# Optimization experiments

Hardware: AMD Instinct MI355X
Metric: run time of the kernel (lower is better)

Reference implementation:

```python
import jax, jax.numpy as jnp
import numpy as np

D_MODEL = 768
D_STATE = 128
D_CONV = 4
EXPAND = 2
HEADDIM = 64
NGROUPS = 1
D_INNER = EXPAND * D_MODEL            # 1536
NHEADS = D_INNER // HEADDIM           # 24
CONV_DIM = D_INNER + 2 * NGROUPS * D_STATE  # 1792
D_IN_PROJ = 2 * D_INNER + 2 * NGROUPS * D_STATE + NHEADS  # 3352
EPS = 1e-5


def setup_inputs() -> dict:
    key = jax.random.key(0)
    ks = jax.random.split(key, 8)
    b, l = 4, 2048
    return {
        "feature": jax.random.normal(ks[0], (b, l, D_MODEL), jnp.float32),
        "in_proj_w": jax.random.normal(ks[1], (D_IN_PROJ, D_MODEL), jnp.float32) * 0.02,
        "conv_w": jax.random.normal(ks[2], (CONV_DIM, D_CONV), jnp.float32) * 0.2,
        "conv_b": jnp.zeros((CONV_DIM,), jnp.float32),
        "dt_bias": jax.random.normal(ks[3], (NHEADS,), jnp.float32) * 0.1,
        # A in [1,16) -> A_log = log(A)
        "A_log": jnp.log(1.0 + 15.0 * jax.random.uniform(ks[4], (NHEADS,), jnp.float32)),
        "D": jnp.ones((NHEADS,), jnp.float32),
        "norm_w": jnp.ones((D_INNER,), jnp.float32),
        "out_proj_w": jax.random.normal(ks[5], (D_MODEL, D_INNER), jnp.float32) * 0.02,
        "gate1": jnp.float32(0.6),
    }


def _mamba2(u, in_proj_w, conv_w, conv_b, dt_bias, A_log, D, norm_w, out_proj_w):
    b, l, _ = u.shape
    zxbcdt = jnp.einsum('bld,ed->ble', u, in_proj_w)  # [b,l,3352]
    z, xBC, dt = jnp.split(zxbcdt, [D_INNER, D_INNER + CONV_DIM], axis=-1)
    dt = jax.nn.softplus(dt + dt_bias)  # [b,l,h]

    # causal depthwise conv1d + silu on xBC
    xc = jnp.transpose(xBC, (0, 2, 1))  # [b,c,l]
    xc = jax.lax.conv_general_dilated(
        xc, conv_w[:, None, :], (1,), [(D_CONV - 1, 0)],
        dimension_numbers=('NCH', 'OIH', 'NCH'), feature_group_count=CONV_DIM)
    xBC = jax.nn.silu(jnp.transpose(xc, (0, 2, 1)) + conv_b)

    x, B, C = jnp.split(xBC, [D_INNER, D_INNER + NGROUPS * D_STATE], axis=-1)
    x = x.reshape(b, l, NHEADS, HEADDIM)
    A = -jnp.exp(A_log)          # [h], negative
    dA = jnp.exp(dt * A)         # [b,l,h]

    def step(h, inp):
        # h: [b,h,p,n]
        dA_t, dt_t, x_t, B_t, C_t = inp  # [b,h],[b,h],[b,h,p],[b,n],[b,n]
        h = h * dA_t[..., None, None] + (dt_t[..., None] * x_t)[..., None] * B_t[:, None, None, :]
        y = jnp.einsum('bhpn,bn->bhp', h, C_t)
        return h, y

    h0 = jnp.zeros((b, NHEADS, HEADDIM, D_STATE), u.dtype)
    xs = (jnp.moveaxis(dA, 1, 0), jnp.moveaxis(dt, 1, 0), jnp.moveaxis(x, 1, 0),
          jnp.moveaxis(B, 1, 0), jnp.moveaxis(C, 1, 0))
    _, ys = jax.lax.scan(step, h0, xs)           # [l,b,h,p]
    y = jnp.moveaxis(ys, 0, 1) + x * D[None, None, :, None]
    y = y.reshape(b, l, D_INNER)

    # gated RMSNorm: gate then normalize (norm_before_gate=False)
    y = y * jax.nn.silu(z)
    y = y * jax.lax.rsqrt(jnp.mean(y * y, axis=-1, keepdims=True) + EPS) * norm_w
    return jnp.einsum('bld,ed->ble', y, out_proj_w)


def reference(feature, in_proj_w, conv_w, conv_b, dt_bias, A_log, D, norm_w, out_proj_w, gate1):
    out = _mamba2(feature, in_proj_w, conv_w, conv_b, dt_bias, A_log, D, norm_w, out_proj_w)
    return jax.nn.sigmoid(gate1) * out
```

## Files before the change

### kernel.cpp

```cpp
#include <hip/hip_runtime.h>
#include <cstddef>

#define NB 4
#define SEQL 2048
#define DMODEL 768
#define DSTATE 128
#define HEADDIM 64
#define NHEADS 24
#define DINNER 1536
#define CONVDIM 1792
#define DINPROJ 3352
#define BLROWS (NB*SEQL)
#define RMS_EPS 1e-5f
#define Q 128
#define NC (SEQL/Q)
#define BOFF DINNER
#define COFF (DINNER + DSTATE)
#define BK 64

typedef unsigned int uint;
typedef unsigned short ushort;
typedef __attribute__((ext_vector_type(8))) short bf16x8;
typedef __attribute__((ext_vector_type(4))) float f32x4;

__device__ __forceinline__ float fexp_(float x){ return __expf(x); }
__device__ __forceinline__ float sigmoidf_(float x){ return 1.f/(1.f+__expf(-x)); }
__device__ __forceinline__ float siluf_(float x){ return x * sigmoidf_(x); }
__device__ __forceinline__ float softplusf_(float x){ return x > 20.f ? x : log1pf(__expf(x)); }

__device__ __forceinline__ ushort f2bf(float f){
    union { float f; uint u; } v; v.f = f;
    uint r = (v.u + 0x7FFFu + ((v.u >> 16) & 1u)) >> 16;
    return (ushort)r;
}
__device__ __forceinline__ float bf2f(ushort s){
    union { uint u; float f; } v; v.u = ((uint)s) << 16;
    return v.f;
}
__device__ __forceinline__ uint pack2(float a, float b){
    return (uint)f2bf(a) | ((uint)f2bf(b) << 16);
}
__device__ __forceinline__ void unpack8(uint4 r, float* o){
    o[0]=bf2f((ushort)(r.x&0xffff)); o[1]=bf2f((ushort)(r.x>>16));
    o[2]=bf2f((ushort)(r.y&0xffff)); o[3]=bf2f((ushort)(r.y>>16));
    o[4]=bf2f((ushort)(r.z&0xffff)); o[5]=bf2f((ushort)(r.z>>16));
    o[6]=bf2f((ushort)(r.w&0xffff)); o[7]=bf2f((ushort)(r.w>>16));
}
__device__ __forceinline__ uint packu2(ushort a, ushort b){
    return (uint)a | ((uint)b << 16);
}

#define GLD16(g, l) __builtin_amdgcn_global_load_lds( \
    (const __attribute__((address_space(1))) void*)(g), \
    (__attribute__((address_space(3))) void*)(l), 16, 0, 0)

#define MFMA_BF16(a, b, c) __builtin_amdgcn_mfma_f32_16x16x32_bf16((a), (b), (c), 0, 0, 0)

__global__ __launch_bounds__(256) void cast2_kernel(
    const float* __restrict__ a, ushort* __restrict__ oa, int n4a,
    const float* __restrict__ b, ushort* __restrict__ ob, int n4b)
{
    const int i = blockIdx.x*256 + threadIdx.x;
    if (i < n4a) {
        float4 v = ((const float4*)a)[i];
        ((ushort4*)oa)[i] = make_ushort4(f2bf(v.x), f2bf(v.y), f2bf(v.z), f2bf(v.w));
    } else {
        const int j = i - n4a;
        if (j < n4b) {
            float4 v = ((const float4*)b)[j];
            ((ushort4*)ob)[j] = make_ushort4(f2bf(v.x), f2bf(v.y), f2bf(v.z), f2bf(v.w));
        }
    }
}

__global__ __launch_bounds__(256) void gemm_mfma(
    const ushort* __restrict__ A, const ushort* __restrict__ W,
    float* __restrict__ C, int M, int N, int K,
    const float* __restrict__ gptr)
{
    __shared__ __align__(16) ushort sm[2*12288];
    const int tid = threadIdx.x;
    const int wv = tid >> 6, ln = tid & 63;
    const int id = blockIdx.x;
    const int xcd = id & 7;
    const int local = id >> 3;
    const int m0 = (xcd*8 + (local & 7)) * 128;
    const int n0 = (local >> 3) * 64;
    const int wm = (wv >> 1) * 64, wn = (wv & 1) * 32;

    const int sr = ln >> 3;
    const int scol = ((ln & 7) ^ sr) * 8;
    const ushort* gA[4]; ushort* lA[4];
#pragma unroll
    for (int iss = 0; iss < 4; ++iss) {
        gA[iss] = A + (size_t)(m0 + wv*32 + iss*8 + sr) * K + scol;
        lA[iss] = &sm[(wv*32 + iss*8) * BK];
    }
    const ushort* gB[2]; ushort* lB[2];
#pragma unroll
    for (int iss = 0; iss < 2; ++iss) {
        gB[iss] = W + (size_t)(n0 + wv*16 + iss*8 + sr) * K + scol;
        lB[iss] = &sm[8192 + (wv*16 + iss*8) * BK];
    }

    f32x4 acc[4][2];
#pragma unroll
    for (int i = 0; i < 4; ++i)
#pragma unroll
        for (int j = 0; j < 2; ++j) acc[i][j] = (f32x4){0.f, 0.f, 0.f, 0.f};

    const int fr = ln & 15;
    const int fq = ln >> 4;
    const int nt = K / BK;

#pragma unroll
    for (int iss = 0; iss < 4; ++iss) GLD16(gA[iss], lA[iss]);
#pragma unroll
    for (int iss = 0; iss < 2; ++iss) GLD16(gB[iss], lB[iss]);

    for (int kt = 0; kt < nt; ++kt) {
        if (kt + 1 < nt) {
            const int so = ((kt + 1) & 1) * 12288;
            const int ko = (kt + 1) * BK;
#pragma unroll
            for (int iss = 0; iss < 4; ++iss) GLD16(gA[iss] + ko, lA[iss] + so);
#pragma unroll
            for (int iss = 0; iss < 2; ++iss) GLD16(gB[iss] + ko, lB[iss] + so);
            asm volatile("s_waitcnt vmcnt(6)" ::: "memory");
        } else {
            asm volatile("s_waitcnt vmcnt(0)" ::: "memory");
        }
        __builtin_amdgcn_s_barrier();
        const ushort* As = sm + (kt & 1) * 12288;
        const ushort* Bs = As + 8192;
#pragma unroll
        for (int kh = 0; kh < 2; ++kh) {
            const int sw = ((kh*4 + fq) ^ (fr & 7)) * 8;
            bf16x8 af[4], bfr[2];
#pragma unroll
            for (int i = 0; i < 4; ++i)
                af[i] = *(const bf16x8*)&As[(wm + i*16 + fr)*BK + sw];
#pragma unroll
            for (int j = 0; j < 2; ++j)
                bfr[j] = *(const bf16x8*)&Bs[(wn + j*16 + fr)*BK + sw];
#pragma unroll
            for (int i = 0; i < 4; ++i)
#pragma unroll
                for (int j = 0; j < 2; ++j)
                    acc[i][j] = MFMA_BF16(af[i], bfr[j], acc[i][j]);
        }
        __builtin_amdgcn_s_barrier();
    }

    float scale = 1.f;
    if (gptr) scale = sigmoidf_(*gptr);
    const int cn = ln & 15;
    const int cr = (ln >> 4) * 4;
#pragma unroll
    for (int i = 0; i < 4; ++i) {
        const int mb = m0 + wm + i*16 + cr;
#pragma unroll
        for (int j = 0; j < 2; ++j) {
            const int n = n0 + wn + j*16 + cn;
            if (n < N) {
                float* cp = C + (size_t)mb * N + n;
                cp[0*(size_t)N] = acc[i][j].x * scale;
                cp[1*(size_t)N] = acc[i][j].y * scale;
                cp[2*(size_t)N] = acc[i][j].z * scale;
                cp[3*(size_t)N] = acc[i][j].w * scale;
            }
        }
    }
}

__global__ __launch_bounds__(256) void gemm_mfma_bf16o(
    const ushort* __restrict__ A, const ushort* __restrict__ W,
    ushort* __restrict__ C, float* __restrict__ dtraw, int M, int N, int K)
{
    __shared__ __align__(16) ushort sm[2*128*BK*2];
    const int tid = threadIdx.x;
    const int wv = tid >> 6, ln = tid & 63;
    const int id = blockIdx.x;
    const int xcd = id & 7;
    const int local = id >> 3;
    const int m0 = (xcd*8 + (local & 7)) * 128;
    const int n0 = (local >> 3) * 128;
    const int wm = (wv >> 1) * 64, wn = (wv & 1) * 64;

    const int sr = ln >> 3;
    const int scol = ((ln & 7) ^ sr) * 8;
    const ushort* gA[4]; const ushort* gB[4];
    ushort* lA[4]; ushort* lB[4];
#pragma unroll
    for (int iss = 0; iss < 4; ++iss) {
        const int ra = m0 + wv*32 + iss*8 + sr;
        gA[iss] = A + (size_t)ra * K + scol;
        int rb = n0 + wv*32 + iss*8 + sr; if (rb >= N) rb = N - 1;
        gB[iss] = W + (size_t)rb * K + scol;
        lA[iss] = &sm[(wv*32 + iss*8) * BK];
        lB[iss] = &sm[8192 + (wv*32 + iss*8) * BK];
    }

    f32x4 acc[4][4];
#pragma unroll
    for (int i = 0; i < 4; ++i)
#pragma unroll
        for (int j = 0; j < 4; ++j) acc[i][j] = (f32x4){0.f, 0.f, 0.f, 0.f};

    const int fr = ln & 15;
    const int fq = ln >> 4;
    const int nt = K / BK;

#pragma unroll
    for (int iss = 0; iss < 4; ++iss) {
        GLD16(gA[iss], lA[iss]);
        GLD16(gB[iss], lB[iss]);
    }

    for (int kt = 0; kt < nt; ++kt) {
        if (kt + 1 < nt) {
            const int so = ((kt + 1) & 1) * 16384;
            const int ko = (kt + 1) * BK;
#pragma unroll
            for (int iss = 0; iss < 4; ++iss) {
                GLD16(gA[iss] + ko, lA[iss] + so);
                GLD16(gB[iss] + ko, lB[iss] + so);
            }
            asm volatile("s_waitcnt vmcnt(8)" ::: "memory");
        } else {
            asm volatile("s_waitcnt vmcnt(0)" ::: "memory");
        }
        __builtin_amdgcn_s_barrier();
        const ushort* As = sm + (kt & 1) * 16384;
        const ushort* Bs = As + 8192;
#pragma unroll
        for (int kh = 0; kh < 2; ++kh) {
            const int sw = ((kh*4 + fq) ^ (fr & 7)) * 8;
            bf16x8 af[4], bfr[4];
#pragma unroll
            for (int i = 0; i < 4; ++i)
                af[i] = *(const bf16x8*)&As[(wm + i*16 + fr)*BK + sw];
#pragma unroll
            for (int j = 0; j < 4; ++j)
                bfr[j] = *(const bf16x8*)&Bs[(wn + j*16 + fr)*BK + sw];
#pragma unroll
            for (int i = 0; i < 4; ++i)
#pragma unroll
                for (int j = 0; j < 4; ++j)
                    acc[i][j] = MFMA_BF16(af[i], bfr[j], acc[i][j]);
        }
        __builtin_amdgcn_s_barrier();
    }

    const int cn = ln & 15;
    const int cr = (ln >> 4) * 4;
    __syncthreads();
    ushort* rp = sm + wv*4096;
#pragma unroll
    for (int i = 0; i < 4; ++i)
#pragma unroll
        for (int j = 0; j < 4; ++j) {
            const int colb = j*16 + cn;
#pragma unroll
            for (int r = 0; r < 4; ++r) {
                const int row = i*16 + cr + r;
                rp[row*64 + (((colb >> 3) ^ (row & 7)) * 8) + (colb & 7)] = f2bf(acc[i][j][r]);
            }
        }
    __syncthreads();
#pragma unroll
    for (int k2 = 0; k2 < 8; ++k2) {
        const int row = k2*8 + (ln >> 3);
        const int cg = ln & 7;
        uint4 v = *(const uint4*)&rp[row*64 + ((cg ^ (row & 7)) * 8)];
        const int gm = m0 + wm + row;
        const int gn = n0 + wn + cg*8;
        if (gn + 8 <= N)
            *(uint4*)(C + (size_t)gm*N + gn) = v;
    }
    if (n0 + 128 > N) {
#pragma unroll
        for (int i = 0; i < 4; ++i) {
            const int mb = m0 + wm + i*16 + cr;
#pragma unroll
            for (int j = 0; j < 4; ++j) {
                const int col = (n0 + wn + j*16 + cn) - (N - 24);
                if (col >= 0 && col < 24) {
                    dtraw[(size_t)(mb+0)*24 + col] = acc[i][j].x;
                    dtraw[(size_t)(mb+1)*24 + col] = acc[i][j].y;
                    dtraw[(size_t)(mb+2)*24 + col] = acc[i][j].z;
                    dtraw[(size_t)(mb+3)*24 + col] = acc[i][j].w;
                }
            }
        }
    }
}

__global__ __launch_bounds__(448) void conv_dtscan_kernel(
    const ushort* __restrict__ zx, const float* __restrict__ conv_w,
    const float* __restrict__ conv_b, ushort* __restrict__ xconv,
    const float* __restrict__ dtraw, const float* __restrict__ dt_bias,
    const float* __restrict__ A_log, float* __restrict__ dtc,
    float* __restrict__ clog)
{
    if (blockIdx.x < BLROWS/16) {
        const int c4 = threadIdx.x;
        const int bl0 = blockIdx.x * 16;
        const int l0 = bl0 & (SEQL - 1);
        float w[4][4];
#pragma unroll
        for (int j = 0; j < 4; ++j) {
            float4 wr = *(const float4*)(conv_w + (c4*4 + j)*4);
            w[j][0]=wr.x; w[j][1]=wr.y; w[j][2]=wr.z; w[j][3]=wr.w;
        }
        const float4 bias = *(const float4*)(conv_b + c4*4);
        const ushort* src = zx + DINNER + (size_t)c4*4;
        ushort* dst = xconv + (size_t)c4*4;

        float h0[4], h1[4], h2[4];
        if (l0 == 0) {
#pragma unroll
            for (int ch = 0; ch < 4; ++ch) { h0[ch]=0.f; h1[ch]=0.f; h2[ch]=0.f; }
        } else {
            ushort4 a = *(const ushort4*)(src + (size_t)(bl0-3)*DINPROJ);
            ushort4 b = *(const ushort4*)(src + (size_t)(bl0-2)*DINPROJ);
            ushort4 c = *(const ushort4*)(src + (size_t)(bl0-1)*DINPROJ);
            h0[0]=bf2f(a.x); h0[1]=bf2f(a.y); h0[2]=bf2f(a.z); h0[3]=bf2f(a.w);
            h1[0]=bf2f(b.x); h1[1]=bf2f(b.y); h1[2]=bf2f(b.z); h1[3]=bf2f(b.w);
            h2[0]=bf2f(c.x); h2[1]=bf2f(c.y); h2[2]=bf2f(c.z); h2[3]=bf2f(c.w);
        }
#pragma unroll
        for (int t = 0; t < 16; ++t) {
            ushort4 xv = *(const ushort4*)(src + (size_t)(bl0 + t)*DINPROJ);
            float h3[4] = {bf2f(xv.x), bf2f(xv.y), bf2f(xv.z), bf2f(xv.w)};
            float s0 = fmaf(h3[0], w[0][3], fmaf(h2[0], w[0][2], fmaf(h1[0], w[0][1], fmaf(h0[0], w[0][0], bias.x))));
            float s1 = fmaf(h3[1], w[1][3], fmaf(h2[1], w[1][2], fmaf(h1[1], w[1][1], fmaf(h0[1], w[1][0], bias.y))));
            float s2 = fmaf(h3[2], w[2][3], fmaf(h2[2], w[2][2], fmaf(h1[2], w[2][1], fmaf(h0[2], w[2][0], bias.z))));
            float s3 = fmaf(h3[3], w[3][3], fmaf(h2[3], w[3][2], fmaf(h1[3], w[3][1], fmaf(h0[3], w[3][0], bias.w))));
            ushort4 o = make_ushort4(f2bf(siluf_(s0)), f2bf(siluf_(s1)),
                                     f2bf(siluf_(s2)), f2bf(siluf_(s3)));
            *(ushort4*)(dst + (size_t)(bl0 + t)*CONVDIM) = o;
#pragma unroll
            for (int ch = 0; ch < 4; ++ch) { h0[ch]=h1[ch]; h1[ch]=h2[ch]; h2[ch]=h3[ch]; }
        }
    } else {
        const int id = blockIdx.x - BLROWS/16;
        const int c = id & (NC - 1);
        const int h = (id >> 4) % NHEADS;
        const int b = id / (NC * NHEADS);
        const int t = threadIdx.x;
        __shared__ float w0tot;
        float v = 0.f, dtv = 0.f;
        if (t < 128) {
            const int bl = b*SEQL + c*Q + t;
            float draw = dtraw[(size_t)bl*24 + h] + dt_bias[h];
            dtv = softplusf_(draw);
            v = -fexp_(A_log[h]) * dtv;
            const int lane = t & 63;
#pragma unroll
            for (int off = 1; off < 64; off <<= 1) {
                float u = __shfl_up(v, off);
                if (lane >= off) v += u;
            }
            if (t == 63) w0tot = v;
        }
        __syncthreads();
        if (t < 128) {
            if (t >= 64) v += w0tot;
            const int idx = (b*NHEADS + h)*SEQL + c*Q + t;
            dtc[idx] = dtv;
            clog[idx] = v;
        }
    }
}

#define ASTR 40
#define BSTR 40
__global__ __launch_bounds__(256) void gcb_locstate_kernel(
    const ushort* __restrict__ xconv, ushort* __restrict__ G,
    const float* __restrict__ dtc, const float* __restrict__ clog,
    ushort* __restrict__ Sloc)
{
    __shared__ __align__(16) char smraw[15872];
    const int tid = threadIdx.x;
    const int wv = tid >> 6, ln = tid & 63;
    const int fr = ln & 15, fq = ln >> 4, fk = fq*8;

    if (blockIdx.x < 2*NC*NB) {
        ushort* Ca = (ushort*)smraw;
        ushort* Bb = (ushort*)(smraw + 4096);
        const int id = blockIdx.x;
        const int thalf = id & 1;
        const int c = (id >> 1) & (NC - 1);
        const int b = id >> 5;
        const int bl0 = b*SEQL + c*Q;
        const int th0 = thalf*64;

        const int sat = tid & 63,  sac = (tid >> 6)*8;
        const int sbt = tid & 127, sbh = (tid >> 7)*16;

        f32x4 acc[4][2];
#pragma unroll
        for (int i = 0; i < 4; ++i)
#pragma unroll
            for (int j = 0; j < 2; ++j) acc[i][j] = (f32x4){0.f,0.f,0.f,0.f};

        for (int ks = 0; ks < 4; ++ks) {
            uint4 av = *(const uint4*)(xconv + (size_t)(bl0 + th0 + sat)*CONVDIM + COFF + ks*32 + sac);
            const ushort* br = xconv + (size_t)(bl0 + sbt)*CONVDIM + BOFF + ks*32 + sbh;
            uint4 bv0 = *(const uint4*)br;
            uint4 bv1 = *(const uint4*)(br + 8);
            __syncthreads();
            *(uint4*)&Ca[sat*32 + sac] = av;
            *(uint4*)&Bb[sbt*32 + sbh] = bv0;
            *(uint4*)&Bb[sbt*32 + sbh + 8] = bv1;
            __syncthreads();
            bf16x8 av_[4], bv_[2];
#pragma unroll
            for (int i = 0; i < 4; ++i)
                av_[i] = *(const bf16x8*)&Ca[(i*16 + fr)*32 + fk];
#pragma unroll
            for (int j = 0; j < 2; ++j)
                bv_[j] = *(const bf16x8*)&Bb[(wv*32 + j*16 + fr)*32 + fk];
#pragma unroll
            for (int i = 0; i < 4; ++i)
#pragma unroll
                for (int j = 0; j < 2; ++j)
                    acc[i][j] = MFMA_BF16(av_[i], bv_[j], acc[i][j]);
        }
        ushort* gout = G + (size_t)(b*NC + c)*(Q*Q);
#pragma unroll
        for (int i = 0; i < 4; ++i) {
#pragma unroll
            for (int j = 0; j < 2; ++j) {
                const int s = wv*32 + j*16 + fr;
#pragma unroll
                for (int r = 0; r < 4; ++r) {
                    const int t = th0 + i*16 + fq*4 + r;
                    gout[t*Q + s] = f2bf(acc[i][j][r]);
                }
            }
        }
    } else {
        ushort* Ab = (ushort*)smraw;
        float* sw = (float*)(smraw + 15360);
        ushort* Bb = (ushort*)(smraw + 5120);
        const int id = blockIdx.x - 2*NC*NB;
        const int c = id & (NC - 1);
        const int h = (id >> 4) % NHEADS;
        const int b = id / (NC * NHEADS);
        const int bh = b*NHEADS + h;
        const int bl0 = b*SEQL + c*Q;

        if (tid < Q) {
            const float ce = clog[(size_t)bh*SEQL + c*Q + (Q-1)];
            const float cs = clog[(size_t)bh*SEQL + c*Q + tid];
            sw[tid] = dtc[(size_t)bh*SEQL + c*Q + tid] * fexp_(ce - cs);
        }

        f32x4 acc[4][2];
#pragma unroll
        for (int i = 0; i < 4; ++i)
#pragma unroll
            for (int j = 0; j < 2; ++j) acc[i][j] = (f32x4){0.f,0.f,0.f,0.f};

        const int ap = tid & 63, aoct = tid >> 6;
        const int bn = tid & 127, bhalf = tid >> 7;

        ushort xrc[8]; ushort buc[16];
#pragma unroll
        for (int j = 0; j < 8; ++j)
            xrc[j] = xconv[(size_t)(bl0 + aoct*8 + j)*CONVDIM + h*HEADDIM + ap];
#pragma unroll
        for (int j = 0; j < 16; ++j)
            buc[j] = xconv[(size_t)(bl0 + bhalf*16 + j)*CONVDIM + BOFF + bn];

        __syncthreads();

        uint4 pkA, pkB0, pkB1;
        {
            float xv[8];
#pragma unroll
            for (int j = 0; j < 8; ++j) xv[j] = bf2f(xrc[j]) * sw[aoct*8 + j];
            pkA = make_uint4(pack2(xv[0],xv[1]), pack2(xv[2],xv[3]),
                             pack2(xv[4],xv[5]), pack2(xv[6],xv[7]));
            pkB0 = make_uint4(packu2(buc[0],buc[1]), packu2(buc[2],buc[3]),
                              packu2(buc[4],buc[5]), packu2(buc[6],buc[7]));
            pkB1 = make_uint4(packu2(buc[8],buc[9]), packu2(buc[10],buc[11]),
                              packu2(buc[12],buc[13]), packu2(buc[14],buc[15]));
        }
#pragma unroll
        for (int j = 0; j < 8; ++j)
            xrc[j] = xconv[(size_t)(bl0 + 32 + aoct*8 + j)*CONVDIM + h*HEADDIM + ap];
#pragma unroll
        for (int j = 0; j < 16; ++j)
            buc[j] = xconv[(size_t)(bl0 + 32 + bhalf*16 + j)*CONVDIM + BOFF + bn];

#pragma unroll
        for (int ks = 0; ks < 4; ++ks) {
            if (ks > 0) __syncthreads();
            *(uint4*)&Ab[ap*ASTR + aoct*8] = pkA;
            *(uint4*)&Bb[bn*BSTR + bhalf*16] = pkB0;
            *(uint4*)&Bb[bn*BSTR + bhalf*16 + 8] = pkB1;
            __syncthreads();
            if (ks < 3) {
                float xv[8];
#pragma unroll
                for (int j = 0; j < 8; ++j) xv[j] = bf2f(xrc[j]) * sw[(ks+1)*32 + aoct*8 + j];
                pkA = make_uint4(pack2(xv[0],xv[1]), pack2(xv[2],xv[3]),
                                 pack2(xv[4],xv[5]), pack2(xv[6],xv[7]));
                pkB0 = make_uint4(packu2(buc[0],buc[1]), packu2(buc[2],buc[3]),
                                  packu2(buc[4],buc[5]), packu2(buc[6],buc[7]));
                pkB1 = make_uint4(packu2(buc[8],buc[9]), packu2(buc[10],buc[11]),
                                  packu2(buc[12],buc[13]), packu2(buc[14],buc[15]));
                if (ks < 2) {
#pragma unroll
                    for (int j = 0; j < 8; ++j)
                        xrc[j] = xconv[(size_t)(bl0 + (ks+2)*32 + aoct*8 + j)*CONVDIM + h*HEADDIM + ap];
#pragma unroll
                    for (int j = 0; j < 16; ++j)
                        buc[j] = xconv[(size_t)(bl0 + (ks+2)*32 + bhalf*16 + j)*CONVDIM + BOFF + bn];
                }
            }
            bf16x8 af[4], bf[2];
#pragma unroll
            for (int i = 0; i < 4; ++i)
                af[i] = *(const bf16x8*)&Ab[(i*16 + fr)*ASTR + fk];
#pragma unroll
            for (int j = 0; j < 2; ++j)
                bf[j] = *(const bf16x8*)&Bb[(wv*32 + j*16 + fr)*BSTR + fk];
#pragma unroll
            for (int i = 0; i < 4; ++i)
#pragma unroll
                for (int j = 0; j < 2; ++j)
                    acc[i][j] = MFMA_BF16(af[i], bf[j], acc[i][j]);
        }
        ushort* dst = Sloc + (size_t)((b*NC + c)*NHEADS + h) * (HEADDIM*DSTATE);
#pragma unroll
        for (int i = 0; i < 4; ++i) {
#pragma unroll
            for (int j = 0; j < 2; ++j) {
                const int n = wv*32 + j*16 + fr;
#pragma unroll
                for (int r = 0; r < 4; ++r) {
                    const int p = i*16 + fq*4 + r;
                    dst[p*DSTATE + n] = f2bf(acc[i][j][r]);
                }
            }
        }
    }
}

__global__ __launch_bounds__(256) void chunkscan_kernel(
    const float* __restrict__ clog, ushort* __restrict__ S)
{
    const int h = blockIdx.x, b = blockIdx.y, pg = blockIdx.z;
    const int tid = threadIdx.x;
    const int p = pg*16 + (tid >> 4);
    const int n0 = (tid & 15) * 8;
    const int bh = b*NHEADS + h;
    float st[8];
#pragma unroll
    for (int j = 0; j < 8; ++j) st[j] = 0.f;

    uint4 raw = *(uint4*)(S + (size_t)((b*NC + 0)*NHEADS + h) * (HEADDIM*DSTATE) + p*DSTATE + n0);
    for (int c = 0; c < NC; ++c) {
        uint4 cur = raw;
        ushort* base = S + (size_t)((b*NC + c)*NHEADS + h) * (HEADDIM*DSTATE);
        if (c + 1 < NC)
            raw = *(uint4*)(S + (size_t)((b*NC + c + 1)*NHEADS + h) * (HEADDIM*DSTATE) + p*DSTATE + n0);
        const float tc = fexp_(clog[(size_t)bh*SEQL + c*Q + (Q-1)]);
        float lv[8];
        unpack8(cur, lv);
        uint4 pre = make_uint4(pack2(st[0],st[1]), pack2(st[2],st[3]),
                               pack2(st[4],st[5]), pack2(st[6],st[7]));
        *(uint4*)(base + p*DSTATE + n0) = pre;
#pragma unroll
        for (int j = 0; j < 8; ++j) st[j] = fmaf(tc, st[j], lv[j]);
    }
}

__global__ __launch_bounds__(256) void ychunk_mfma(
    const ushort* __restrict__ xconv, const float* __restrict__ dtc,
    const float* __restrict__ clog, const ushort* __restrict__ G,
    const ushort* __restrict__ Sp, const float* __restrict__ Dv,
    ushort* __restrict__ ybf)
{
    __shared__ __align__(16) ushort smu[8192];
    ushort* Ab = smu;
    ushort* Bb = smu + 4096;
    __shared__ float s_clog[Q];
    __shared__ float s_dtc[Q];
    const int c = blockIdx.x, h = blockIdx.y, b = blockIdx.z;
    const int tid = threadIdx.x;
    const int wv = tid >> 6, ln = tid & 63;
    const int bh = b*NHEADS + h;
    const int bl0 = b*SEQL + c*Q;
    const int fr = ln & 15, fq = ln >> 4, fk = fq*8;

    if (tid < Q) {
        s_clog[tid] = clog[(size_t)bh*SEQL + c*Q + tid];
        s_dtc[tid]  = dtc [(size_t)bh*SEQL + c*Q + tid];
    }

    f32x4 acc[2][4];
#pragma unroll
    for (int i = 0; i < 2; ++i)
#pragma unroll
        for (int j = 0; j < 4; ++j) acc[i][j] = (f32x4){0.f,0.f,0.f,0.f};

    const int sgt = tid & 127, sgh = (tid >> 7)*16;
    const int sbp = tid & 63,  sbc = (tid >> 6)*8;
    const ushort* spb = Sp + (size_t)((b*NC + c)*NHEADS + h)*(HEADDIM*DSTATE);

    uint4 cv0c = *(const uint4*)(xconv + (size_t)(bl0 + sgt)*CONVDIM + COFF + sgh);
    uint4 cv1c = *(const uint4*)(xconv + (size_t)(bl0 + sgt)*CONVDIM + COFF + sgh + 8);
    uint4 svc  = *(const uint4*)(spb + sbp*DSTATE + sbc);
#pragma unroll
    for (int ks = 0; ks < 4; ++ks) {
        __syncthreads();
        *(uint4*)&Ab[sgt*32 + sgh]     = cv0c;
        *(uint4*)&Ab[sgt*32 + sgh + 8] = cv1c;
        *(uint4*)&Bb[sbp*32 + sbc] = svc;
        if (ks < 3) {
            const ushort* cr = xconv + (size_t)(bl0 + sgt)*CONVDIM + COFF + (ks+1)*32 + sgh;
            cv0c = *(const uint4*)cr;
            cv1c = *(const uint4*)(cr + 8);
            svc  = *(const uint4*)(spb + sbp*DSTATE + (ks+1)*32 + sbc);
        }
        __syncthreads();
        bf16x8 af[2], bv[4];
        af[0] = *(const bf16x8*)&Ab[(wv*32 +      fr)*32 + fk];
        af[1] = *(const bf16x8*)&Ab[(wv*32 + 16 + fr)*32 + fk];
#pragma unroll
        for (int j = 0; j < 4; ++j)
            bv[j] = *(const bf16x8*)&Bb[(j*16 + fr)*32 + fk];
#pragma unroll
        for (int i = 0; i < 2; ++i)
#pragma unroll
            for (int j = 0; j < 4; ++j)
                acc[i][j] = MFMA_BF16(af[i], bv[j], acc[i][j]);
    }

    const ushort* gp = G + (size_t)(b*NC + c)*(Q*Q);
    uint4 g0c = *(const uint4*)(gp + sgt*Q + sgh);
    uint4 g1c = *(const uint4*)(gp + sgt*Q + sgh + 8);
    ushort xuc[8];
#pragma unroll
    for (int j = 0; j < 8; ++j)
        xuc[j] = xconv[(size_t)(bl0 + sbc + j)*CONVDIM + h*HEADDIM + sbp];

#pragma unroll
    for (int i = 0; i < 2; ++i) {
        const int tb = wv*32 + i*16 + fq*4;
        float e0 = fexp_(s_clog[tb+0]), e1 = fexp_(s_clog[tb+1]);
        float e2 = fexp_(s_clog[tb+2]), e3 = fexp_(s_clog[tb+3]);
#pragma unroll
        for (int j = 0; j < 4; ++j) {
            acc[i][j].x *= e0; acc[i][j].y *= e1; acc[i][j].z *= e2; acc[i][j].w *= e3;
        }
    }

    const float ct = s_clog[sgt];

    uint4 pkA0, pkA1, pkB;
#define YPK(KS) do { \
        float gvals[16]; \
        unpack8(g0c, gvals); \
        unpack8(g1c, gvals + 8); \
        ushort gw[16]; \
        _Pragma("unroll") \
        for (int j = 0; j < 16; ++j) { \
            const int s = (KS)*32 + sgh + j; \
            float w = 0.f; \
            if (s <= sgt) w = s_dtc[s] * fexp_(ct - s_clog[s]); \
            gw[j] = f2bf(gvals[j] * w); \
        } \
        pkA0 = make_uint4(packu2(gw[0],gw[1]), packu2(gw[2],gw[3]), \
                          packu2(gw[4],gw[5]), packu2(gw[6],gw[7])); \
        pkA1 = make_uint4(packu2(gw[8],gw[9]), packu2(gw[10],gw[11]), \
                          packu2(gw[12],gw[13]), packu2(gw[14],gw[15])); \
        pkB  = make_uint4(packu2(xuc[0],xuc[1]), packu2(xuc[2],xuc[3]), \
                          packu2(xuc[4],xuc[5]), packu2(xuc[6],xuc[7])); \
    } while (0)

    YPK(0);
    g0c = *(const uint4*)(gp + sgt*Q + 32 + sgh);
    g1c = *(const uint4*)(gp + sgt*Q + 32 + sgh + 8);
#pragma unroll
    for (int j = 0; j < 8; ++j)
        xuc[j] = xconv[(size_t)(bl0 + 32 + sbc + j)*CONVDIM + h*HEADDIM + sbp];

#pragma unroll
    for (int ks = 0; ks < 4; ++ks) {
        __syncthreads();
        *(uint4*)&Ab[sgt*32 + sgh]     = pkA0;
        *(uint4*)&Ab[sgt*32 + sgh + 8] = pkA1;
        *(uint4*)&Bb[sbp*32 + sbc]     = pkB;
        __syncthreads();
        if (ks < 3) {
            YPK(ks+1);
            if (ks < 2) {
                g0c = *(const uint4*)(gp + sgt*Q + (ks+2)*32 + sgh);
                g1c = *(const uint4*)(gp + sgt*Q + (ks+2)*32 + sgh + 8);
#pragma unroll
                for (int j = 0; j < 8; ++j)
                    xuc[j] = xconv[(size_t)(bl0 + (ks+2)*32 + sbc + j)*CONVDIM + h*HEADDIM + sbp];
            }
        }
        if (ks <= wv) {
            bf16x8 af[2], bv[4];
            af[0] = *(const bf16x8*)&Ab[(wv*32 +      fr)*32 + fk];
            af[1] = *(const bf16x8*)&Ab[(wv*32 + 16 + fr)*32 + fk];
#pragma unroll
            for (int j = 0; j < 4; ++j)
                bv[j] = *(const bf16x8*)&Bb[(j*16 + fr)*32 + fk];
#pragma unroll
            for (int i = 0; i < 2; ++i)
#pragma unroll
                for (int j = 0; j < 4; ++j)
                    acc[i][j] = MFMA_BF16(af[i], bv[j], acc[i][j]);
        }
    }
#undef YPK

    const float Dh = Dv[h];
    __syncthreads();
    ushort* rp = smu;
#pragma unroll
    for (int i = 0; i < 2; ++i) {
#pragma unroll
        for (int r = 0; r < 4; ++r) {
            const int t = wv*32 + i*16 + fq*4 + r;
            const ushort* xr = xconv + (size_t)(bl0 + t)*CONVDIM + h*HEADDIM;
#pragma unroll
            for (int j = 0; j < 4; ++j) {
                const int p = j*16 + fr;
                rp[t*64 + p] = f2bf(acc[i][j][r] + Dh * bf2f(xr[p]));
            }
        }
    }
#pragma unroll
    for (int k2 = 0; k2 < 4; ++k2) {
        const int row = wv*32 + k2*8 + (ln >> 3);
        uint4 v = *(const uint4*)&rp[row*64 + (ln & 7)*8];
        *(uint4*)(ybf + (size_t)(bl0 + row)*DINNER + h*HEADDIM + (ln & 7)*8) = v;
    }
}

__global__ __launch_bounds__(128) void rms_cast_kernel(
    const ushort* __restrict__ zx, const float* __restrict__ norm_w,
    ushort* __restrict__ ybf, const float* __restrict__ wout,
    ushort* __restrict__ wout_bf)
{
    const int tid = threadIdx.x;
    if (blockIdx.x < BLROWS) {
        const int row = blockIdx.x;
        const ushort* zr = zx + (size_t)row * DINPROJ;
        ushort* yr = ybf + (size_t)row * DINNER;
        float v[12];
        float ss = 0.f;
#pragma unroll
        for (int i = 0; i < 3; ++i) {
            const int o = (tid + i*128) * 4;
            ushort4 yv = *(const ushort4*)(yr + o);
            ushort4 zv = *(const ushort4*)(zr + o);
            float a = bf2f(yv.x) * siluf_(bf2f(zv.x));
            float b = bf2f(yv.y) * siluf_(bf2f(zv.y));
            float cc = bf2f(yv.z) * siluf_(bf2f(zv.z));
            float d = bf2f(yv.w) * siluf_(bf2f(zv.w));
            v[i*4+0]=a; v[i*4+1]=b; v[i*4+2]=cc; v[i*4+3]=d;
            ss += a*a + b*b + cc*cc + d*d;
        }
#pragma unroll
        for (int off = 1; off < 64; off <<= 1) ss += __shfl_xor(ss, off);
        __shared__ float red[2];
        if ((tid & 63) == 0) red[tid >> 6] = ss;
        __syncthreads();
        const float rstd = rsqrtf((red[0] + red[1]) * (1.f/DINNER) + RMS_EPS);
#pragma unroll
        for (int i = 0; i < 3; ++i) {
            const int o = (tid + i*128) * 4;
            float4 wv = *(const float4*)(norm_w + o);
            ushort4 ov = make_ushort4(f2bf(v[i*4+0]*rstd*wv.x), f2bf(v[i*4+1]*rstd*wv.y),
                                      f2bf(v[i*4+2]*rstd*wv.z), f2bf(v[i*4+3]*rstd*wv.w));
            *(ushort4*)(yr + o) = ov;
        }
    } else {
        const int i = (blockIdx.x - BLROWS)*128 + tid;
        const int n4 = DMODEL*DINNER/4;
        if (i < n4) {
            float4 v = ((const float4*)wout)[i];
            ((ushort4*)wout_bf)[i] = make_ushort4(f2bf(v.x), f2bf(v.y), f2bf(v.z), f2bf(v.w));
        }
    }
}

extern "C" void kernel_launch(void* const* d_in, const int* in_sizes, int n_in,
                              void* d_out, int out_size, void* d_ws, size_t ws_size,
                              hipStream_t stream)
{
    const float* feature    = (const float*)d_in[0];
    const float* in_proj_w  = (const float*)d_in[1];
    const float* conv_w     = (const float*)d_in[2];
    const float* conv_b     = (const float*)d_in[3];
    const float* dt_bias    = (const float*)d_in[4];
    const float* A_log      = (const float*)d_in[5];
    const float* Dvec       = (const float*)d_in[6];
    const float* norm_w     = (const float*)d_in[7];
    const float* out_proj_w = (const float*)d_in[8];
    const float* gate1      = (const float*)d_in[9];
    float* out = (float*)d_out;

    ushort* zx    = (ushort*)d_ws;
    ushort* xconv = zx + (size_t)BLROWS * DINPROJ;
    ushort* ybf   = xconv + (size_t)BLROWS * CONVDIM;
    float* dtraw  = (float*)(ybf + (size_t)BLROWS * DINNER);
    float* dtc    = dtraw + (size_t)BLROWS * 24;
    float* clog   = dtc + (size_t)NB * NHEADS * SEQL;
    ushort* Gbuf  = (ushort*)(clog + (size_t)NB * NHEADS * SEQL);
    ushort* Sbuf  = Gbuf + (size_t)NB * NC * Q * Q;
    ushort* Abf    = Gbuf;
    ushort* Wbf_in = Gbuf + (size_t)BLROWS * DMODEL;
    ushort* Wbf_out = Sbuf;

    const int n4a = BLROWS*DMODEL/4;
    const int n4b = DINPROJ*DMODEL/4;
    cast2_kernel<<<dim3((n4a + n4b + 255)/256), 256, 0, stream>>>(
        feature, Abf, n4a, in_proj_w, Wbf_in, n4b);
    gemm_mfma_bf16o<<<dim3(27*64), 256, 0, stream>>>(Abf, Wbf_in, zx, dtraw,
                                                     BLROWS, DINPROJ, DMODEL);
    conv_dtscan_kernel<<<dim3(BLROWS/16 + NB*NHEADS*NC), 448, 0, stream>>>(
        zx, conv_w, conv_b, xconv, dtraw, dt_bias, A_log, dtc, clog);
    gcb_locstate_kernel<<<dim3(2*NC*NB + NC*NHEADS*NB), 256, 0, stream>>>(
        xconv, Gbuf, dtc, clog, Sbuf);
    chunkscan_kernel<<<dim3(NHEADS, NB, 4), 256, 0, stream>>>(clog, Sbuf);
    ychunk_mfma<<<dim3(NC, NHEADS, NB), 256, 0, stream>>>(xconv, dtc, clog, Gbuf, Sbuf, Dvec, ybf);
    rms_cast_kernel<<<dim3(BLROWS + (DMODEL*DINNER/4 + 127)/128), 128, 0, stream>>>(
        zx, norm_w, ybf, out_proj_w, Wbf_out);
    gemm_mfma<<<dim3(768), 256, 0, stream>>>(ybf, Wbf_out, out,
                                             BLROWS, DMODEL, DINNER, gate1);
}
```

Baseline: 262.0 us.

## Fuse inter-chunk state scan into local-state kernel via last-block atomic counter

Removes the separate chunkscan kernel launch. Each (batch, head) keeps an atomic counter, and the last chunk block to finish runs the sequential scan across chunks over all 64 rows. The counter is zeroed in the cast kernel and lives in the ybf buffer, which is only written later. This saves a launch and overlaps the scan with other blocks' work, but the scan now runs on only 96 blocks with a 4x larger per-thread workload, plus fences and atomics.

Measured after the change: 655.1 us. 2.5x slower.

```diff
diff --git a/kernel.cpp b/kernel.cpp
--- a/kernel.cpp
+++ b/kernel.cpp
@@ -58,9 +58,11 @@
 
 __global__ __launch_bounds__(256) void cast2_kernel(
     const float* __restrict__ a, ushort* __restrict__ oa, int n4a,
-    const float* __restrict__ b, ushort* __restrict__ ob, int n4b)
+    const float* __restrict__ b, ushort* __restrict__ ob, int n4b,
+    uint* __restrict__ cnt)
 {
     const int i = blockIdx.x*256 + threadIdx.x;
+    if (blockIdx.x == 0 && threadIdx.x < NB*NHEADS) cnt[threadIdx.x] = 0u;
     if (i < n4a) {
         float4 v = ((const float4*)a)[i];
         ((ushort4*)oa)[i] = make_ushort4(f2bf(v.x), f2bf(v.y), f2bf(v.z), f2bf(v.w));
@@ -379,7 +381,7 @@
 __global__ __launch_bounds__(256) void gcb_locstate_kernel(
     const ushort* __restrict__ xconv, ushort* __restrict__ G,
     const float* __restrict__ dtc, const float* __restrict__ clog,
-    ushort* __restrict__ Sloc)
+    ushort* __restrict__ Sloc, uint* __restrict__ cnt)
 {
     __shared__ __align__(16) char smraw[15872];
     const int tid = threadIdx.x;
@@ -445,6 +447,7 @@
         ushort* Ab = (ushort*)smraw;
         float* sw = (float*)(smraw + 15360);
         ushort* Bb = (ushort*)(smraw + 5120);
+        __shared__ uint is_last;
         const int id = blockIdx.x - 2*NC*NB;
         const int c = id & (NC - 1);
         const int h = (id >> 4) % NHEADS;
@@ -548,35 +551,54 @@
                 }
             }
         }
-    }
-}
-
-__global__ __launch_bounds__(256) void chunkscan_kernel(
-    const float* __restrict__ clog, ushort* __restrict__ S)
-{
-    const int h = blockIdx.x, b = blockIdx.y, pg = blockIdx.z;
-    const int tid = threadIdx.x;
-    const int p = pg*16 + (tid >> 4);
-    const int n0 = (tid & 15) * 8;
-    const int bh = b*NHEADS + h;
-    float st[8];
-#pragma unroll
-    for (int j = 0; j < 8; ++j) st[j] = 0.f;
-
-    uint4 raw = *(uint4*)(S + (size_t)((b*NC + 0)*NHEADS + h) * (HEADDIM*DSTATE) + p*DSTATE + n0);
-    for (int c = 0; c < NC; ++c) {
-        uint4 cur = raw;
-        ushort* base = S + (size_t)((b*NC + c)*NHEADS + h) * (HEADDIM*DSTATE);
-        if (c + 1 < NC)
-            raw = *(uint4*)(S + (size_t)((b*NC + c + 1)*NHEADS + h) * (HEADDIM*DSTATE) + p*DSTATE + n0);
-        const float tc = fexp_(clog[(size_t)bh*SEQL + c*Q + (Q-1)]);
-        float lv[8];
-        unpack8(cur, lv);
-        uint4 pre = make_uint4(pack2(st[0],st[1]), pack2(st[2],st[3]),
-                               pack2(st[4],st[5]), pack2(st[6],st[7]));
-        *(uint4*)(base + p*DSTATE + n0) = pre;
-#pragma unroll
-        for (int j = 0; j < 8; ++j) st[j] = fmaf(tc, st[j], lv[j]);
+
+        __threadfence();
+        __syncthreads();
+        if (tid == 0)
+            is_last = (atomicAdd(&cnt[bh], 1u) == (uint)(NC - 1));
+        __syncthreads();
+        if (is_last) {
+            __threadfence();
+            const int pr = tid >> 4;
+            const int n0 = (tid & 15) * 8;
+            float st[4][8];
+#pragma unroll
+            for (int pg = 0; pg < 4; ++pg)
+#pragma unroll
+                for (int j = 0; j < 8; ++j) st[pg][j] = 0.f;
+
+            uint4 nxt[4];
+            {
+                ushort* base0 = Sloc + (size_t)((b*NC + 0)*NHEADS + h) * (HEADDIM*DSTATE);
+#pragma unroll
+                for (int pg = 0; pg < 4; ++pg)
+                    nxt[pg] = *(uint4*)(base0 + (pg*16 + pr)*DSTATE + n0);
+            }
+            for (int cc = 0; cc < NC; ++cc) {
+                uint4 cur[4];
+#pragma unroll
+                for (int pg = 0; pg < 4; ++pg) cur[pg] = nxt[pg];
+                ushort* base = Sloc + (size_t)((b*NC + cc)*NHEADS + h) * (HEADDIM*DSTATE);
+                if (cc + 1 < NC) {
+                    ushort* bn_ = Sloc + (size_t)((b*NC + cc + 1)*NHEADS + h) * (HEADDIM*DSTATE);
+#pragma unroll
+                    for (int pg = 0; pg < 4; ++pg)
+                        nxt[pg] = *(uint4*)(bn_ + (pg*16 + pr)*DSTATE + n0);
+                }
+                const float tc = fexp_(clog[(size_t)bh*SEQL + cc*Q + (Q-1)]);
+#pragma unroll
+                for (int pg = 0; pg < 4; ++pg) {
+                    float lv[8];
+                    unpack8(cur[pg], lv);
+                    uint4 pre = make_uint4(pack2(st[pg][0],st[pg][1]), pack2(st[pg][2],st[pg][3]),
+                                           pack2(st[pg][4],st[pg][5]), pack2(st[pg][6],st[pg][7]));
+                    *(uint4*)(base + (pg*16 + pr)*DSTATE + n0) = pre;
+#pragma unroll
+                    for (int j = 0; j < 8; ++j) st[pg][j] = fmaf(tc, st[pg][j], lv[j]);
+                }
+            }
+            __threadfence();
+        }
     }
 }
 
@@ -823,18 +845,18 @@
     ushort* Abf    = Gbuf;
     ushort* Wbf_in = Gbuf + (size_t)BLROWS * DMODEL;
     ushort* Wbf_out = Sbuf;
+    uint* cnt = (uint*)ybf;
 
     const int n4a = BLROWS*DMODEL/4;
     const int n4b = DINPROJ*DMODEL/4;
     cast2_kernel<<<dim3((n4a + n4b + 255)/256), 256, 0, stream>>>(
-        feature, Abf, n4a, in_proj_w, Wbf_in, n4b);
+        feature, Abf, n4a, in_proj_w, Wbf_in, n4b, cnt);
     gemm_mfma_bf16o<<<dim3(27*64), 256, 0, stream>>>(Abf, Wbf_in, zx, dtraw,
                                                      BLROWS, DINPROJ, DMODEL);
     conv_dtscan_kernel<<<dim3(BLROWS/16 + NB*NHEADS*NC), 448, 0, stream>>>(
         zx, conv_w, conv_b, xconv, dtraw, dt_bias, A_log, dtc, clog);
     gcb_locstate_kernel<<<dim3(2*NC*NB + NC*NHEADS*NB), 256, 0, stream>>>(
-        xconv, Gbuf, dtc, clog, Sbuf);
-    chunkscan_kernel<<<dim3(NHEADS, NB, 4), 256, 0, stream>>>(clog, Sbuf);
+        xconv, Gbuf, dtc, clog, Sbuf, cnt);
     ychunk_mfma<<<dim3(NC, NHEADS, NB), 256, 0, stream>>>(xconv, dtc, clog, Gbuf, Sbuf, Dvec, ybf);
     rms_cast_kernel<<<dim3(BLROWS + (DMODEL*DINNER/4 + 127)/128), 128, 0, stream>>>(
         zx, norm_w, ybf, out_proj_w, Wbf_out);
```

## Split in-proj GEMM and overlap z-columns GEMM with conv and dt scan

Applied to the files above, without the earlier changes.

The input projection GEMM is split in two. The first launch computes only the xBC and dt columns. A second fused kernel then runs the z-column GEMM tiles alongside the conv1d+SiLU and dt cumsum blocks, which depend only on the first launch. This is meant to fill the device with independent work and hide the memory-bound conv and scan under GEMM compute. The conv blocks are halved to 224 active threads to fit a 256-thread launch, and the fused kernel carries the GEMM's large shared allocation for every block, which may reduce occupancy for the conv and scan blocks.

Measured after the change: 269.1 us. +2.7%, slower.

```diff
diff --git a/kernel.cpp b/kernel.cpp
--- a/kernel.cpp
+++ b/kernel.cpp
@@ -17,6 +17,10 @@
 #define BOFF DINNER
 #define COFF (DINNER + DSTATE)
 #define BK 64
+#define N_XBCDT 1816
+#define NB_G1B (12*64)
+#define NB_CONV ((BLROWS/16)*2)
+#define NB_DT (NB*NHEADS*NC)
 
 typedef unsigned int uint;
 typedef unsigned short ushort;
@@ -173,14 +177,13 @@
     }
 }
 
-__global__ __launch_bounds__(256) void gemm_mfma_bf16o(
-    const ushort* __restrict__ A, const ushort* __restrict__ W,
-    ushort* __restrict__ C, float* __restrict__ dtraw, int M, int N, int K)
-{
-    __shared__ __align__(16) ushort sm[2*128*BK*2];
+__device__ __forceinline__ void gemm_bf16o_dev(
+    ushort* sm, const ushort* __restrict__ A, const ushort* __restrict__ W,
+    ushort* __restrict__ C, float* __restrict__ dtraw,
+    int N, int K, int ldc, int id)
+{
     const int tid = threadIdx.x;
     const int wv = tid >> 6, ln = tid & 63;
-    const int id = blockIdx.x;
     const int xcd = id & 7;
     const int local = id >> 3;
     const int m0 = (xcd*8 + (local & 7)) * 128;
@@ -276,9 +279,9 @@
         const int gm = m0 + wm + row;
         const int gn = n0 + wn + cg*8;
         if (gn + 8 <= N)
-            *(uint4*)(C + (size_t)gm*N + gn) = v;
-    }
-    if (n0 + 128 > N) {
+            *(uint4*)(C + (size_t)gm*ldc + gn) = v;
+    }
+    if (dtraw && n0 + 128 > N) {
 #pragma unroll
         for (int i = 0; i < 4; ++i) {
             const int mb = m0 + wm + i*16 + cr;
@@ -296,60 +299,78 @@
     }
 }
 
-__global__ __launch_bounds__(448) void conv_dtscan_kernel(
-    const ushort* __restrict__ zx, const float* __restrict__ conv_w,
-    const float* __restrict__ conv_b, ushort* __restrict__ xconv,
+__global__ __launch_bounds__(256) void gemm_mfma_bf16o(
+    const ushort* __restrict__ A, const ushort* __restrict__ W,
+    ushort* __restrict__ C, float* __restrict__ dtraw, int N, int K, int ldc)
+{
+    __shared__ __align__(16) ushort sm[2*128*BK*2];
+    gemm_bf16o_dev(sm, A, W, C, dtraw, N, K, ldc, blockIdx.x);
+}
+
+__global__ __launch_bounds__(256) void gemmz_conv_dtscan_kernel(
+    const ushort* __restrict__ Abf, const ushort* __restrict__ Wbf,
+    ushort* __restrict__ zx,
+    const float* __restrict__ conv_w, const float* __restrict__ conv_b,
+    ushort* __restrict__ xconv,
     const float* __restrict__ dtraw, const float* __restrict__ dt_bias,
     const float* __restrict__ A_log, float* __restrict__ dtc,
     float* __restrict__ clog)
 {
-    if (blockIdx.x < BLROWS/16) {
-        const int c4 = threadIdx.x;
-        const int bl0 = blockIdx.x * 16;
-        const int l0 = bl0 & (SEQL - 1);
-        float w[4][4];
-#pragma unroll
-        for (int j = 0; j < 4; ++j) {
-            float4 wr = *(const float4*)(conv_w + (c4*4 + j)*4);
-            w[j][0]=wr.x; w[j][1]=wr.y; w[j][2]=wr.z; w[j][3]=wr.w;
-        }
-        const float4 bias = *(const float4*)(conv_b + c4*4);
-        const ushort* src = zx + DINNER + (size_t)c4*4;
-        ushort* dst = xconv + (size_t)c4*4;
-
-        float h0[4], h1[4], h2[4];
-        if (l0 == 0) {
-#pragma unroll
-            for (int ch = 0; ch < 4; ++ch) { h0[ch]=0.f; h1[ch]=0.f; h2[ch]=0.f; }
-        } else {
-            ushort4 a = *(const ushort4*)(src + (size_t)(bl0-3)*DINPROJ);
-            ushort4 b = *(const ushort4*)(src + (size_t)(bl0-2)*DINPROJ);
-            ushort4 c = *(const ushort4*)(src + (size_t)(bl0-1)*DINPROJ);
-            h0[0]=bf2f(a.x); h0[1]=bf2f(a.y); h0[2]=bf2f(a.z); h0[3]=bf2f(a.w);
-            h1[0]=bf2f(b.x); h1[1]=bf2f(b.y); h1[2]=bf2f(b.z); h1[3]=bf2f(b.w);
-            h2[0]=bf2f(c.x); h2[1]=bf2f(c.y); h2[2]=bf2f(c.z); h2[3]=bf2f(c.w);
-        }
-#pragma unroll
-        for (int t = 0; t < 16; ++t) {
-            ushort4 xv = *(const ushort4*)(src + (size_t)(bl0 + t)*DINPROJ);
-            float h3[4] = {bf2f(xv.x), bf2f(xv.y), bf2f(xv.z), bf2f(xv.w)};
-            float s0 = fmaf(h3[0], w[0][3], fmaf(h2[0], w[0][2], fmaf(h1[0], w[0][1], fmaf(h0[0], w[0][0], bias.x))));
-            float s1 = fmaf(h3[1], w[1][3], fmaf(h2[1], w[1][2], fmaf(h1[1], w[1][1], fmaf(h0[1], w[1][0], bias.y))));
-            float s2 = fmaf(h3[2], w[2][3], fmaf(h2[2], w[2][2], fmaf(h1[2], w[2][1], fmaf(h0[2], w[2][0], bias.z))));
-            float s3 = fmaf(h3[3], w[3][3], fmaf(h2[3], w[3][2], fmaf(h1[3], w[3][1], fmaf(h0[3], w[3][0], bias.w))));
-            ushort4 o = make_ushort4(f2bf(siluf_(s0)), f2bf(siluf_(s1)),
-                                     f2bf(siluf_(s2)), f2bf(siluf_(s3)));
-            *(ushort4*)(dst + (size_t)(bl0 + t)*CONVDIM) = o;
-#pragma unroll
-            for (int ch = 0; ch < 4; ++ch) { h0[ch]=h1[ch]; h1[ch]=h2[ch]; h2[ch]=h3[ch]; }
+    __shared__ __align__(16) ushort sm[2*128*BK*2];
+    if (blockIdx.x < NB_G1B) {
+        gemm_bf16o_dev(sm, Abf, Wbf, zx, nullptr, DINNER, DMODEL, DINPROJ, blockIdx.x);
+    } else if (blockIdx.x < NB_G1B + NB_CONV) {
+        const int cid = blockIdx.x - NB_G1B;
+        const int bl0 = (cid >> 1) * 16;
+        const int chalf = cid & 1;
+        const int tid = threadIdx.x;
+        if (tid < 224) {
+            const int c4 = chalf*224 + tid;
+            const int l0 = bl0 & (SEQL - 1);
+            float w[4][4];
+#pragma unroll
+            for (int j = 0; j < 4; ++j) {
+                float4 wr = *(const float4*)(conv_w + (c4*4 + j)*4);
+                w[j][0]=wr.x; w[j][1]=wr.y; w[j][2]=wr.z; w[j][3]=wr.w;
+            }
+            const float4 bias = *(const float4*)(conv_b + c4*4);
+            const ushort* src = zx + DINNER + (size_t)c4*4;
+            ushort* dst = xconv + (size_t)c4*4;
+
+            float h0[4], h1[4], h2[4];
+            if (l0 == 0) {
+#pragma unroll
+                for (int ch = 0; ch < 4; ++ch) { h0[ch]=0.f; h1[ch]=0.f; h2[ch]=0.f; }
+            } else {
+                ushort4 a = *(const ushort4*)(src + (size_t)(bl0-3)*DINPROJ);
+                ushort4 b = *(const ushort4*)(src + (size_t)(bl0-2)*DINPROJ);
+                ushort4 c = *(const ushort4*)(src + (size_t)(bl0-1)*DINPROJ);
+                h0[0]=bf2f(a.x); h0[1]=bf2f(a.y); h0[2]=bf2f(a.z); h0[3]=bf2f(a.w);
+                h1[0]=bf2f(b.x); h1[1]=bf2f(b.y); h1[2]=bf2f(b.z); h1[3]=bf2f(b.w);
+                h2[0]=bf2f(c.x); h2[1]=bf2f(c.y); h2[2]=bf2f(c.z); h2[3]=bf2f(c.w);
+            }
+#pragma unroll
+            for (int t = 0; t < 16; ++t) {
+                ushort4 xv = *(const ushort4*)(src + (size_t)(bl0 + t)*DINPROJ);
+                float h3[4] = {bf2f(xv.x), bf2f(xv.y), bf2f(xv.z), bf2f(xv.w)};
+                float s0 = fmaf(h3[0], w[0][3], fmaf(h2[0], w[0][2], fmaf(h1[0], w[0][1], fmaf(h0[0], w[0][0], bias.x))));
+                float s1 = fmaf(h3[1], w[1][3], fmaf(h2[1], w[1][2], fmaf(h1[1], w[1][1], fmaf(h0[1], w[1][0], bias.y))));
+                float s2 = fmaf(h3[2], w[2][3], fmaf(h2[2], w[2][2], fmaf(h1[2], w[2][1], fmaf(h0[2], w[2][0], bias.z))));
+                float s3 = fmaf(h3[3], w[3][3], fmaf(h2[3], w[3][2], fmaf(h1[3], w[3][1], fmaf(h0[3], w[3][0], bias.w))));
+                ushort4 o = make_ushort4(f2bf(siluf_(s0)), f2bf(siluf_(s1)),
+                                         f2bf(siluf_(s2)), f2bf(siluf_(s3)));
+                *(ushort4*)(dst + (size_t)(bl0 + t)*CONVDIM) = o;
+#pragma unroll
+                for (int ch = 0; ch < 4; ++ch) { h0[ch]=h1[ch]; h1[ch]=h2[ch]; h2[ch]=h3[ch]; }
+            }
         }
     } else {
-        const int id = blockIdx.x - BLROWS/16;
+        const int id = blockIdx.x - (NB_G1B + NB_CONV);
         const int c = id & (NC - 1);
         const int h = (id >> 4) % NHEADS;
         const int b = id / (NC * NHEADS);
         const int t = threadIdx.x;
-        __shared__ float w0tot;
+        float* w0tot = (float*)sm;
         float v = 0.f, dtv = 0.f;
         if (t < 128) {
             const int bl = b*SEQL + c*Q + t;
@@ -362,11 +383,11 @@
                 float u = __shfl_up(v, off);
                 if (lane >= off) v += u;
             }
-            if (t == 63) w0tot = v;
+            if (t == 63) w0tot[0] = v;
         }
         __syncthreads();
         if (t < 128) {
-            if (t >= 64) v += w0tot;
+            if (t >= 64) v += w0tot[0];
             const int idx = (b*NHEADS + h)*SEQL + c*Q + t;
             dtc[idx] = dtv;
             clog[idx] = v;
@@ -828,10 +849,11 @@
     const int n4b = DINPROJ*DMODEL/4;
     cast2_kernel<<<dim3((n4a + n4b + 255)/256), 256, 0, stream>>>(
         feature, Abf, n4a, in_proj_w, Wbf_in, n4b);
-    gemm_mfma_bf16o<<<dim3(27*64), 256, 0, stream>>>(Abf, Wbf_in, zx, dtraw,
-                                                     BLROWS, DINPROJ, DMODEL);
-    conv_dtscan_kernel<<<dim3(BLROWS/16 + NB*NHEADS*NC), 448, 0, stream>>>(
-        zx, conv_w, conv_b, xconv, dtraw, dt_bias, A_log, dtc, clog);
+    gemm_mfma_bf16o<<<dim3(15*64), 256, 0, stream>>>(
+        Abf, Wbf_in + (size_t)DINNER*DMODEL, zx + DINNER, dtraw,
+        N_XBCDT, DMODEL, DINPROJ);
+    gemmz_conv_dtscan_kernel<<<dim3(NB_G1B + NB_CONV + NB_DT), 256, 0, stream>>>(
+        Abf, Wbf_in, zx, conv_w, conv_b, xconv, dtraw, dt_bias, A_log, dtc, clog);
     gcb_locstate_kernel<<<dim3(2*NC*NB + NC*NHEADS*NB), 256, 0, stream>>>(
         xconv, Gbuf, dtc, clog, Sbuf);
     chunkscan_kernel<<<dim3(NHEADS, NB, 4), 256, 0, stream>>>(clog, Sbuf);
```
